# Optimization experiments

Measured on AMD Instinct MI355X. Metric: run time of the kernel, lower is better.

## Reference

```python
import jax, jax.numpy as jnp
import numpy as np

N = 100000        # nodes
E = 3200000       # edges (avg degree 32)
D_IN, D_H, D_OUT = 128, 128, 64
EPS = 1e-5        # BatchNorm eps


def setup_inputs() -> dict:
    key = jax.random.key(0)
    ks = jax.random.split(key, 12)
    s = 0.1
    return {
        "x": jax.random.normal(ks[0], (N, D_IN), jnp.float32),
        "edge_index": jax.random.randint(ks[1], (2, E), 0, N, jnp.int32),
        "W1": jax.random.normal(ks[2], (D_IN, D_H), jnp.float32) * s,
        "b1": jnp.zeros((D_H,), jnp.float32),
        "W2": jax.random.normal(ks[3], (D_H, D_H), jnp.float32) * s,
        "b2": jnp.zeros((D_H,), jnp.float32),
        "W3": jax.random.normal(ks[4], (D_H, D_OUT), jnp.float32) * s,
        "b3": jnp.zeros((D_OUT,), jnp.float32),
        "g1": jnp.ones((D_H,), jnp.float32),
        "be1": jnp.zeros((D_H,), jnp.float32),
        "g2": jnp.ones((D_H,), jnp.float32),
        "be2": jnp.zeros((D_H,), jnp.float32),
    }


def reference(x, edge_index, W1, b1, W2, b2, W3, b3, g1, be1, g2, be2):
    # GCNConv normalization: add self-loops, symmetric deg^-1/2 A deg^-1/2
    loop = jnp.arange(N, dtype=edge_index.dtype)
    src = jnp.concatenate([edge_index[0], loop])   # [E+N]
    dst = jnp.concatenate([edge_index[1], loop])   # [E+N]
    deg = jax.ops.segment_sum(jnp.ones(src.shape, x.dtype), dst, num_segments=N)
    dinv = jnp.where(deg > 0, jax.lax.rsqrt(deg), 0.0)
    norm = (dinv[src] * dinv[dst])[:, None]        # [E+N, 1]

    def conv(h, W, b):
        h = h @ W                                   # dense transform [N, d]
        msg = h[src] * norm                         # gather + scale [E+N, d]
        return jax.ops.segment_sum(msg, dst, num_segments=N) + b

    def bn(h, g, be):  # BatchNorm1d over nodes (batch stats, eval-style dropout)
        m = h.mean(axis=0)
        v = h.var(axis=0)
        return (h - m) * jax.lax.rsqrt(v + EPS) * g + be

    h = jax.nn.relu(bn(conv(x, W1, b1), g1, be1))
    h = jax.nn.relu(bn(conv(h, W2, b2), g2, be2))
    h = conv(h, W3, b3)
    return jax.nn.softmax(h, axis=1)
```

## Files before the change

### kernel.cpp

```cpp
#include <hip/hip_runtime.h>
#include <hip/hip_fp16.h>

constexpr int   NN   = 100000;
constexpr int   NE   = 3200000;
constexpr float BN_EPS = 1e-5f;

typedef _Float16 half8 __attribute__((ext_vector_type(8)));
typedef float    floatx16 __attribute__((ext_vector_type(16)));

__global__ __launch_bounds__(256) void k_count(const int* __restrict__ dst,
                                               int* __restrict__ deg,
                                               int* __restrict__ slot) {
  int e = blockIdx.x * 256 + threadIdx.x;
  if (e < NE) slot[e] = atomicAdd(&deg[dst[e]], 1);
}

__global__ __launch_bounds__(256) void k_scan_a(const int* __restrict__ deg,
                                                float* __restrict__ dinv,
                                                int* __restrict__ rowptr,
                                                int* __restrict__ bsum) {
  __shared__ int sd[256];
  int t = threadIdx.x;
  int i = blockIdx.x * 256 + t;
  int v = (i < NN) ? deg[i] : 0;
  if (i < NN) dinv[i] = rsqrtf((float)(v + 1));
  sd[t] = v;
  __syncthreads();
  for (int off = 1; off < 256; off <<= 1) {
    int x = (t >= off) ? sd[t - off] : 0;
    __syncthreads();
    sd[t] += x;
    __syncthreads();
  }
  if (i < NN) rowptr[i] = sd[t] - v;
  if (t == 255) bsum[blockIdx.x] = sd[255];
}

__global__ __launch_bounds__(512) void k_scan_b(int* __restrict__ bsum, int nb) {
  __shared__ int sd[512];
  int t = threadIdx.x;
  int v = (t < nb) ? bsum[t] : 0;
  sd[t] = v;
  __syncthreads();
  for (int off = 1; off < 512; off <<= 1) {
    int x = (t >= off) ? sd[t - off] : 0;
    __syncthreads();
    sd[t] += x;
    __syncthreads();
  }
  if (t < nb) bsum[t] = sd[t] - v;
}

__global__ __launch_bounds__(256) void k_scan_c(int* __restrict__ rowptr,
                                                const int* __restrict__ bsum) {
  int i = blockIdx.x * 256 + threadIdx.x;
  if (i < NN) rowptr[i] += bsum[blockIdx.x];
  if (i == 0) rowptr[NN] = NE;
}

__global__ __launch_bounds__(256) void k_fill(const int* __restrict__ ei,
                                              const int* __restrict__ rowptr,
                                              const int* __restrict__ slot,
                                              int* __restrict__ csrc) {
  int e = blockIdx.x * 256 + threadIdx.x;
  if (e >= NE) return;
  int s = ei[e];
  int d = ei[NE + e];
  csrc[rowptr[d] + slot[e]] = s;
}

template <int BN_>
__global__ __launch_bounds__(256) void k_wprep(const float* __restrict__ W,
                                               _Float16* __restrict__ Wt) {
  int idx = blockIdx.x * 256 + threadIdx.x;
  if (idx >= 128 * BN_) return;
  int k = idx / BN_, n = idx % BN_;
  Wt[n * 128 + k] = (_Float16)W[idx];
}

template <int BN_, bool FUSE_BN>
__global__ __launch_bounds__(256) void k_mgemm(const float* __restrict__ A,
                                               const _Float16* __restrict__ Wt,
                                               const float* __restrict__ scale,
                                               const float* __restrict__ shift,
                                               const float* __restrict__ dinv,
                                               _Float16* __restrict__ C) {
  constexpr int NCT = BN_ / 32;
  int wid  = (blockIdx.x * 256 + threadIdx.x) >> 6;
  int lane = threadIdx.x & 63;
  if (wid >= NN / 32) return;
  const int m = lane & 31;
  const int q = lane >> 5;
  const int row0 = wid * 32;

  const float* Arow = A + (size_t)(row0 + m) * 128 + q * 8;

  floatx16 acc[NCT] = {};

#pragma unroll
  for (int s = 0; s < 8; ++s) {
    float4 a0 = *(const float4*)(Arow + 16 * s);
    float4 a1 = *(const float4*)(Arow + 16 * s + 4);
    if (FUSE_BN) {
      int k0 = 16 * s + q * 8;
      float4 sc0 = *(const float4*)(scale + k0);
      float4 sc1 = *(const float4*)(scale + k0 + 4);
      float4 sh0 = *(const float4*)(shift + k0);
      float4 sh1 = *(const float4*)(shift + k0 + 4);
      a0.x = fmaxf(fmaf(a0.x, sc0.x, sh0.x), 0.f);
      a0.y = fmaxf(fmaf(a0.y, sc0.y, sh0.y), 0.f);
      a0.z = fmaxf(fmaf(a0.z, sc0.z, sh0.z), 0.f);
      a0.w = fmaxf(fmaf(a0.w, sc0.w, sh0.w), 0.f);
      a1.x = fmaxf(fmaf(a1.x, sc1.x, sh1.x), 0.f);
      a1.y = fmaxf(fmaf(a1.y, sc1.y, sh1.y), 0.f);
      a1.z = fmaxf(fmaf(a1.z, sc1.z, sh1.z), 0.f);
      a1.w = fmaxf(fmaf(a1.w, sc1.w, sh1.w), 0.f);
    }
    half8 af;
    af[0] = (_Float16)a0.x; af[1] = (_Float16)a0.y;
    af[2] = (_Float16)a0.z; af[3] = (_Float16)a0.w;
    af[4] = (_Float16)a1.x; af[5] = (_Float16)a1.y;
    af[6] = (_Float16)a1.z; af[7] = (_Float16)a1.w;
#pragma unroll
    for (int ct = 0; ct < NCT; ++ct) {
      half8 bf = *(const half8*)(Wt + (size_t)(ct * 32 + m) * 128 + q * 8 + 16 * s);
      acc[ct] = __builtin_amdgcn_mfma_f32_32x32x16_f16(af, bf, acc[ct], 0, 0, 0);
    }
  }

#pragma unroll
  for (int ct = 0; ct < NCT; ++ct) {
#pragma unroll
    for (int r = 0; r < 16; ++r) {
      int row = (r & 3) + 8 * (r >> 2) + 4 * q;
      float dv = dinv[row0 + row];
      C[(size_t)(row0 + row) * BN_ + ct * 32 + m] = (_Float16)(acc[ct][r] * dv);
    }
  }
}

__global__ __launch_bounds__(256) void k_agg128(const __half* __restrict__ H,
                                                const float* __restrict__ dinv,
                                                const int* __restrict__ rowptr,
                                                const int* __restrict__ srcs,
                                                float* __restrict__ out) {
  int wid  = (blockIdx.x * 256 + threadIdx.x) >> 6;
  int lane = threadIdx.x & 63;
  if (wid >= NN) return;
  const __half2* Hp = (const __half2*)H;
  float2 acc = __half22float2(Hp[(size_t)wid * 64 + lane]);
  int beg = rowptr[wid], end = rowptr[wid + 1];
  int e = beg;
  int end8 = beg + ((end - beg) & ~7);
  for (; e < end8; e += 8) {
    __half2 v0 = Hp[(size_t)srcs[e+0] * 64 + lane];
    __half2 v1 = Hp[(size_t)srcs[e+1] * 64 + lane];
    __half2 v2 = Hp[(size_t)srcs[e+2] * 64 + lane];
    __half2 v3 = Hp[(size_t)srcs[e+3] * 64 + lane];
    __half2 v4 = Hp[(size_t)srcs[e+4] * 64 + lane];
    __half2 v5 = Hp[(size_t)srcs[e+5] * 64 + lane];
    __half2 v6 = Hp[(size_t)srcs[e+6] * 64 + lane];
    __half2 v7 = Hp[(size_t)srcs[e+7] * 64 + lane];
    float2 f0 = __half22float2(v0), f1 = __half22float2(v1);
    float2 f2 = __half22float2(v2), f3 = __half22float2(v3);
    float2 f4 = __half22float2(v4), f5 = __half22float2(v5);
    float2 f6 = __half22float2(v6), f7 = __half22float2(v7);
    acc.x += (f0.x + f1.x) + (f2.x + f3.x) + (f4.x + f5.x) + (f6.x + f7.x);
    acc.y += (f0.y + f1.y) + (f2.y + f3.y) + (f4.y + f5.y) + (f6.y + f7.y);
  }
  for (; e < end; ++e) {
    float2 f = __half22float2(Hp[(size_t)srcs[e] * 64 + lane]);
    acc.x += f.x; acc.y += f.y;
  }
  float di = dinv[wid];
  acc.x *= di; acc.y *= di;
  ((float2*)out)[(size_t)wid * 64 + lane] = acc;
}

__global__ __launch_bounds__(256) void k_agg64_softmax(const __half* __restrict__ H,
                                                       const float* __restrict__ dinv,
                                                       const int* __restrict__ rowptr,
                                                       const int* __restrict__ srcs,
                                                       const float* __restrict__ b3,
                                                       float* __restrict__ out) {
  int wid  = (blockIdx.x * 256 + threadIdx.x) >> 6;
  int lane = threadIdx.x & 63;
  if (wid >= NN) return;
  float acc = __half2float(H[(size_t)wid * 64 + lane]);
  int beg = rowptr[wid], end = rowptr[wid + 1];
  int e = beg;
  int end8 = beg + ((end - beg) & ~7);
  for (; e < end8; e += 8) {
    float v0 = __half2float(H[(size_t)srcs[e+0] * 64 + lane]);
    float v1 = __half2float(H[(size_t)srcs[e+1] * 64 + lane]);
    float v2 = __half2float(H[(size_t)srcs[e+2] * 64 + lane]);
    float v3 = __half2float(H[(size_t)srcs[e+3] * 64 + lane]);
    float v4 = __half2float(H[(size_t)srcs[e+4] * 64 + lane]);
    float v5 = __half2float(H[(size_t)srcs[e+5] * 64 + lane]);
    float v6 = __half2float(H[(size_t)srcs[e+6] * 64 + lane]);
    float v7 = __half2float(H[(size_t)srcs[e+7] * 64 + lane]);
    acc += (v0 + v1) + (v2 + v3) + (v4 + v5) + (v6 + v7);
  }
  for (; e < end; ++e)
    acc += __half2float(H[(size_t)srcs[e] * 64 + lane]);
  acc = acc * dinv[wid] + b3[lane];

  float m = acc;
#pragma unroll
  for (int off = 32; off > 0; off >>= 1) m = fmaxf(m, __shfl_xor(m, off));
  float ev = __expf(acc - m);
  float s = ev;
#pragma unroll
  for (int off = 32; off > 0; off >>= 1) s += __shfl_xor(s, off);
  out[(size_t)wid * 64 + lane] = ev / s;
}

__global__ __launch_bounds__(256) void k_stats(const float* __restrict__ H,
                                               float* __restrict__ S1,
                                               float* __restrict__ S2) {
  int t = threadIdx.x;
  int col  = t & 127;
  int half = t >> 7;
  float s1 = 0.f, s2 = 0.f;
  for (int row = blockIdx.x * 2 + half; row < NN; row += gridDim.x * 2) {
    float v = H[(size_t)row * 128 + col];
    s1 += v; s2 += v * v;
  }
  __shared__ float l1[256], l2[256];
  l1[t] = s1; l2[t] = s2;
  __syncthreads();
  if (t < 128) {
    atomicAdd(&S1[col], l1[t] + l1[t + 128]);
    atomicAdd(&S2[col], l2[t] + l2[t + 128]);
  }
}

__global__ void k_finalize(const float* __restrict__ S1, const float* __restrict__ S2,
                           const float* __restrict__ g,  const float* __restrict__ be,
                           float* __restrict__ scale,    float* __restrict__ shift) {
  int t = threadIdx.x;
  float mean = S1[t] * (1.0f / NN);
  float var  = S2[t] * (1.0f / NN) - mean * mean;
  float is   = rsqrtf(var + BN_EPS);
  float sc   = g[t] * is;
  scale[t] = sc;
  shift[t] = be[t] - mean * sc;
}

extern "C" void kernel_launch(void* const* d_in, const int* in_sizes, int n_in,
                              void* d_out, int out_size, void* d_ws, size_t ws_size,
                              hipStream_t stream) {
  (void)in_sizes; (void)n_in; (void)out_size; (void)ws_size;
  const float* x   = (const float*)d_in[0];
  const int*   ei  = (const int*)d_in[1];
  const float* W1  = (const float*)d_in[2];
  const float* W2  = (const float*)d_in[4];
  const float* W3  = (const float*)d_in[6];
  const float* b3  = (const float*)d_in[7];
  const float* g1  = (const float*)d_in[8];
  const float* be1 = (const float*)d_in[9];
  const float* g2  = (const float*)d_in[10];
  const float* be2 = (const float*)d_in[11];
  float* out = (float*)d_out;

  char* ws = (char*)d_ws;
  size_t off = 0;
  auto take = [&](size_t bytes) -> char* {
    char* p = ws + off;
    off = (off + bytes + 255) & ~(size_t)255;
    return p;
  };
  int*   deg    = (int*)  take((size_t)NN * 4);
  float* S1a    = (float*)take(128 * 4);
  float* S2a    = (float*)take(128 * 4);
  float* S1b    = (float*)take(128 * 4);
  float* S2b    = (float*)take(128 * 4);
  size_t zero_bytes = off;
  float* scale1 = (float*)take(128 * 4);
  float* shift1 = (float*)take(128 * 4);
  float* scale2 = (float*)take(128 * 4);
  float* shift2 = (float*)take(128 * 4);
  float* dinv   = (float*)take((size_t)NN * 4);
  int*   rowptr = (int*)  take((size_t)(NN + 1) * 4);
  int*   bsum   = (int*)  take(1024 * 4);
  int*   slot   = (int*)  take((size_t)NE * 4);
  int*   csrc   = (int*)  take((size_t)NE * 4);
  _Float16* Wt1 = (_Float16*)take((size_t)128 * 128 * 2);
  _Float16* Wt2 = (_Float16*)take((size_t)128 * 128 * 2);
  _Float16* Wt3 = (_Float16*)take((size_t)64 * 128 * 2);
  _Float16* Hf  = (_Float16*)take((size_t)NN * 128 * 2);
  float*    bufB= (float*)   take((size_t)NN * 128 * 4);

  (void)hipMemsetAsync(d_ws, 0, zero_bytes, stream);

  const int nbE = (NE + 255) / 256;
  const int nbN = (NN + 255) / 256;
  const int mgB = (NN / 32 + 3) / 4;
  const int aggB  = (NN + 3) / 4;

  k_count <<<nbE, 256, 0, stream>>>(ei + NE, deg, slot);
  k_scan_a<<<nbN, 256, 0, stream>>>(deg, dinv, rowptr, bsum);
  k_scan_b<<<1, 512, 0, stream>>>(bsum, nbN);
  k_scan_c<<<nbN, 256, 0, stream>>>(rowptr, bsum);
  k_fill  <<<nbE, 256, 0, stream>>>(ei, rowptr, slot, csrc);

  k_wprep<128><<<64, 256, 0, stream>>>(W1, Wt1);
  k_wprep<128><<<64, 256, 0, stream>>>(W2, Wt2);
  k_wprep<64> <<<32, 256, 0, stream>>>(W3, Wt3);

  k_mgemm<128, false><<<mgB, 256, 0, stream>>>(x, Wt1, nullptr, nullptr, dinv, Hf);
  k_agg128<<<aggB, 256, 0, stream>>>((const __half*)Hf, dinv, rowptr, csrc, bufB);
  k_stats<<<1024, 256, 0, stream>>>(bufB, S1a, S2a);
  k_finalize<<<1, 128, 0, stream>>>(S1a, S2a, g1, be1, scale1, shift1);

  k_mgemm<128, true><<<mgB, 256, 0, stream>>>(bufB, Wt2, scale1, shift1, dinv, Hf);
  k_agg128<<<aggB, 256, 0, stream>>>((const __half*)Hf, dinv, rowptr, csrc, bufB);
  k_stats<<<1024, 256, 0, stream>>>(bufB, S1b, S2b);
  k_finalize<<<1, 128, 0, stream>>>(S1b, S2b, g2, be2, scale2, shift2);

  k_mgemm<64, true><<<mgB, 256, 0, stream>>>(bufB, Wt3, scale2, shift2, dinv, Hf);
  k_agg64_softmax<<<aggB, 256, 0, stream>>>((const __half*)Hf, dinv, rowptr, csrc, b3, out);
}
```

Measured before the change: 842.4 us.

## Store aggregated hidden features in fp16 and pack degree counters into bytes

The aggregation kernel now writes its normalized output as fp16 instead of fp32. The BatchNorm stats kernel and the fused-BN GEMM read that fp16 buffer, which halves the memory traffic of the intermediate activations across both layers. Degree counting now uses byte-packed counters, four nodes per 32-bit word, which shrinks the zeroed region and the atomic footprint. The cost is extra fp16 rounding before BatchNorm, and node degrees above 255 would silently overflow.

Result: slower. 874.5 us (+3.8%).

```diff
diff --git a/kernel.cpp b/kernel.cpp
--- a/kernel.cpp
+++ b/kernel.cpp
@@ -9,20 +9,24 @@
 typedef float    floatx16 __attribute__((ext_vector_type(16)));
 
 __global__ __launch_bounds__(256) void k_count(const int* __restrict__ dst,
-                                               int* __restrict__ deg,
+                                               unsigned* __restrict__ degp,
                                                int* __restrict__ slot) {
   int e = blockIdx.x * 256 + threadIdx.x;
-  if (e < NE) slot[e] = atomicAdd(&deg[dst[e]], 1);
-}
-
-__global__ __launch_bounds__(256) void k_scan_a(const int* __restrict__ deg,
+  if (e >= NE) return;
+  int d = dst[e];
+  unsigned sh = (d & 3) * 8;
+  unsigned old = atomicAdd(&degp[d >> 2], 1u << sh);
+  slot[e] = (old >> sh) & 0xFF;
+}
+
+__global__ __launch_bounds__(256) void k_scan_a(const unsigned* __restrict__ degp,
                                                 float* __restrict__ dinv,
                                                 int* __restrict__ rowptr,
                                                 int* __restrict__ bsum) {
   __shared__ int sd[256];
   int t = threadIdx.x;
   int i = blockIdx.x * 256 + t;
-  int v = (i < NN) ? deg[i] : 0;
+  int v = (i < NN) ? (int)((degp[i >> 2] >> (8 * (i & 3))) & 0xFF) : 0;
   if (i < NN) dinv[i] = rsqrtf((float)(v + 1));
   sd[t] = v;
   __syncthreads();
@@ -78,8 +82,8 @@
   Wt[n * 128 + k] = (_Float16)W[idx];
 }
 
-template <int BN_, bool FUSE_BN>
-__global__ __launch_bounds__(256) void k_mgemm(const float* __restrict__ A,
+template <int BN_, bool FUSE_BN, typename AT>
+__global__ __launch_bounds__(256) void k_mgemm(const AT* __restrict__ A,
                                                const _Float16* __restrict__ Wt,
                                                const float* __restrict__ scale,
                                                const float* __restrict__ shift,
@@ -93,34 +97,32 @@
   const int q = lane >> 5;
   const int row0 = wid * 32;
 
-  const float* Arow = A + (size_t)(row0 + m) * 128 + q * 8;
+  const AT* Arow = A + (size_t)(row0 + m) * 128 + q * 8;
 
   floatx16 acc[NCT] = {};
 
 #pragma unroll
   for (int s = 0; s < 8; ++s) {
-    float4 a0 = *(const float4*)(Arow + 16 * s);
-    float4 a1 = *(const float4*)(Arow + 16 * s + 4);
+    float av[8];
+    if constexpr (__is_same(AT, float)) {
+      float4 a0 = *(const float4*)(Arow + 16 * s);
+      float4 a1 = *(const float4*)(Arow + 16 * s + 4);
+      av[0] = a0.x; av[1] = a0.y; av[2] = a0.z; av[3] = a0.w;
+      av[4] = a1.x; av[5] = a1.y; av[6] = a1.z; av[7] = a1.w;
+    } else {
+      half8 raw = *(const half8*)(Arow + 16 * s);
+#pragma unroll
+      for (int j = 0; j < 8; ++j) av[j] = (float)raw[j];
+    }
     if (FUSE_BN) {
       int k0 = 16 * s + q * 8;
-      float4 sc0 = *(const float4*)(scale + k0);
-      float4 sc1 = *(const float4*)(scale + k0 + 4);
-      float4 sh0 = *(const float4*)(shift + k0);
-      float4 sh1 = *(const float4*)(shift + k0 + 4);
-      a0.x = fmaxf(fmaf(a0.x, sc0.x, sh0.x), 0.f);
-      a0.y = fmaxf(fmaf(a0.y, sc0.y, sh0.y), 0.f);
-      a0.z = fmaxf(fmaf(a0.z, sc0.z, sh0.z), 0.f);
-      a0.w = fmaxf(fmaf(a0.w, sc0.w, sh0.w), 0.f);
-      a1.x = fmaxf(fmaf(a1.x, sc1.x, sh1.x), 0.f);
-      a1.y = fmaxf(fmaf(a1.y, sc1.y, sh1.y), 0.f);
-      a1.z = fmaxf(fmaf(a1.z, sc1.z, sh1.z), 0.f);
-      a1.w = fmaxf(fmaf(a1.w, sc1.w, sh1.w), 0.f);
+#pragma unroll
+      for (int j = 0; j < 8; ++j)
+        av[j] = fmaxf(fmaf(av[j], scale[k0 + j], shift[k0 + j]), 0.f);
     }
     half8 af;
-    af[0] = (_Float16)a0.x; af[1] = (_Float16)a0.y;
-    af[2] = (_Float16)a0.z; af[3] = (_Float16)a0.w;
-    af[4] = (_Float16)a1.x; af[5] = (_Float16)a1.y;
-    af[6] = (_Float16)a1.z; af[7] = (_Float16)a1.w;
+#pragma unroll
+    for (int j = 0; j < 8; ++j) af[j] = (_Float16)av[j];
 #pragma unroll
     for (int ct = 0; ct < NCT; ++ct) {
       half8 bf = *(const half8*)(Wt + (size_t)(ct * 32 + m) * 128 + q * 8 + 16 * s);
@@ -143,7 +145,7 @@
                                                 const float* __restrict__ dinv,
                                                 const int* __restrict__ rowptr,
                                                 const int* __restrict__ srcs,
-                                                float* __restrict__ out) {
+                                                __half2* __restrict__ out) {
   int wid  = (blockIdx.x * 256 + threadIdx.x) >> 6;
   int lane = threadIdx.x & 63;
   if (wid >= NN) return;
@@ -173,8 +175,7 @@
     acc.x += f.x; acc.y += f.y;
   }
   float di = dinv[wid];
-  acc.x *= di; acc.y *= di;
-  ((float2*)out)[(size_t)wid * 64 + lane] = acc;
+  out[(size_t)wid * 64 + lane] = __floats2half2_rn(acc.x * di, acc.y * di);
 }
 
 __global__ __launch_bounds__(256) void k_agg64_softmax(const __half* __restrict__ H,
@@ -215,23 +216,33 @@
   out[(size_t)wid * 64 + lane] = ev / s;
 }
 
-__global__ __launch_bounds__(256) void k_stats(const float* __restrict__ H,
+__global__ __launch_bounds__(256) void k_stats(const __half2* __restrict__ H2,
                                                float* __restrict__ S1,
                                                float* __restrict__ S2) {
   int t = threadIdx.x;
-  int col  = t & 127;
-  int half = t >> 7;
-  float s1 = 0.f, s2 = 0.f;
-  for (int row = blockIdx.x * 2 + half; row < NN; row += gridDim.x * 2) {
-    float v = H[(size_t)row * 128 + col];
-    s1 += v; s2 += v * v;
-  }
-  __shared__ float l1[256], l2[256];
+  int p = t & 63;
+  int r = t >> 6;
+  float2 s1 = {0.f, 0.f}, s2 = {0.f, 0.f};
+  for (int row = blockIdx.x * 4 + r; row < NN; row += gridDim.x * 4) {
+    float2 v = __half22float2(H2[(size_t)row * 64 + p]);
+    s1.x += v.x; s1.y += v.y;
+    s2.x += v.x * v.x; s2.y += v.y * v.y;
+  }
+  __shared__ float2 l1[256], l2[256];
   l1[t] = s1; l2[t] = s2;
   __syncthreads();
   if (t < 128) {
-    atomicAdd(&S1[col], l1[t] + l1[t + 128]);
-    atomicAdd(&S2[col], l2[t] + l2[t + 128]);
+    l1[t].x += l1[t+128].x; l1[t].y += l1[t+128].y;
+    l2[t].x += l2[t+128].x; l2[t].y += l2[t+128].y;
+  }
+  __syncthreads();
+  if (t < 64) {
+    float2 a1 = l1[t], b1 = l1[t+64];
+    float2 a2 = l2[t], b2 = l2[t+64];
+    atomicAdd(&S1[2*p+0], a1.x + b1.x);
+    atomicAdd(&S1[2*p+1], a1.y + b1.y);
+    atomicAdd(&S2[2*p+0], a2.x + b2.x);
+    atomicAdd(&S2[2*p+1], a2.y + b2.y);
   }
 }
 
@@ -270,7 +281,7 @@
     off = (off + bytes + 255) & ~(size_t)255;
     return p;
   };
-  int*   deg    = (int*)  take((size_t)NN * 4);
+  unsigned* degp = (unsigned*)take((size_t)(NN / 4) * 4);
   float* S1a    = (float*)take(128 * 4);
   float* S2a    = (float*)take(128 * 4);
   float* S1b    = (float*)take(128 * 4);
@@ -289,7 +300,7 @@
   _Float16* Wt2 = (_Float16*)take((size_t)128 * 128 * 2);
   _Float16* Wt3 = (_Float16*)take((size_t)64 * 128 * 2);
   _Float16* Hf  = (_Float16*)take((size_t)NN * 128 * 2);
-  float*    bufB= (float*)   take((size_t)NN * 128 * 4);
+  _Float16* hB  = (_Float16*)take((size_t)NN * 128 * 2);
 
   (void)hipMemsetAsync(d_ws, 0, zero_bytes, stream);
 
@@ -298,8 +309,8 @@
   const int mgB = (NN / 32 + 3) / 4;
   const int aggB  = (NN + 3) / 4;
 
-  k_count <<<nbE, 256, 0, stream>>>(ei + NE, deg, slot);
-  k_scan_a<<<nbN, 256, 0, stream>>>(deg, dinv, rowptr, bsum);
+  k_count <<<nbE, 256, 0, stream>>>(ei + NE, degp, slot);
+  k_scan_a<<<nbN, 256, 0, stream>>>(degp, dinv, rowptr, bsum);
   k_scan_b<<<1, 512, 0, stream>>>(bsum, nbN);
   k_scan_c<<<nbN, 256, 0, stream>>>(rowptr, bsum);
   k_fill  <<<nbE, 256, 0, stream>>>(ei, rowptr, slot, csrc);
@@ -308,16 +319,16 @@
   k_wprep<128><<<64, 256, 0, stream>>>(W2, Wt2);
   k_wprep<64> <<<32, 256, 0, stream>>>(W3, Wt3);
 
-  k_mgemm<128, false><<<mgB, 256, 0, stream>>>(x, Wt1, nullptr, nullptr, dinv, Hf);
-  k_agg128<<<aggB, 256, 0, stream>>>((const __half*)Hf, dinv, rowptr, csrc, bufB);
-  k_stats<<<1024, 256, 0, stream>>>(bufB, S1a, S2a);
+  k_mgemm<128, false, float><<<mgB, 256, 0, stream>>>(x, Wt1, nullptr, nullptr, dinv, Hf);
+  k_agg128<<<aggB, 256, 0, stream>>>((const __half*)Hf, dinv, rowptr, csrc, (__half2*)hB);
+  k_stats<<<1024, 256, 0, stream>>>((const __half2*)hB, S1a, S2a);
   k_finalize<<<1, 128, 0, stream>>>(S1a, S2a, g1, be1, scale1, shift1);
 
-  k_mgemm<128, true><<<mgB, 256, 0, stream>>>(bufB, Wt2, scale1, shift1, dinv, Hf);
-  k_agg128<<<aggB, 256, 0, stream>>>((const __half*)Hf, dinv, rowptr, csrc, bufB);
-  k_stats<<<1024, 256, 0, stream>>>(bufB, S1b, S2b);
+  k_mgemm<128, true, _Float16><<<mgB, 256, 0, stream>>>(hB, Wt2, scale1, shift1, dinv, Hf);
+  k_agg128<<<aggB, 256, 0, stream>>>((const __half*)Hf, dinv, rowptr, csrc, (__half2*)hB);
+  k_stats<<<1024, 256, 0, stream>>>((const __half2*)hB, S1b, S2b);
   k_finalize<<<1, 128, 0, stream>>>(S1b, S2b, g2, be2, scale2, shift2);
 
-  k_mgemm<64, true><<<mgB, 256, 0, stream>>>(bufB, Wt3, scale2, shift2, dinv, Hf);
+  k_mgemm<64, true, _Float16><<<mgB, 256, 0, stream>>>(hB, Wt3, scale2, shift2, dinv, Hf);
   k_agg64_softmax<<<aggB, 256, 0, stream>>>((const __half*)Hf, dinv, rowptr, csrc, b3, out);
 }
```
